# Kernel optimization log

Measured on AMD Instinct MI355X. Metric: run time of the kernel, lower is better.

Reference implementation:

```python
import jax, jax.numpy as jnp
import numpy as np

N = 100000   # nodes
E = 1200000  # edges
D = 64       # feat_dim == num_hidden
G = 64       # graphs in batch
EPS = 1e-5   # BatchNorm eps


def setup_inputs() -> dict:
    key = jax.random.key(0)
    ks = jax.random.split(key, 24)
    inp = {}
    inp['x'] = jax.random.normal(ks[0], (N, D), jnp.float32)
    inp['edge_index'] = jax.random.randint(ks[1], (2, E), 0, N, dtype=jnp.int32)
    inp['batch'] = jnp.sort(jax.random.randint(ks[2], (N,), 0, G, dtype=jnp.int32))
    s = 1.0 / np.sqrt(D)
    for i, kw in zip(range(1, 4), ks[3:6]):
        inp[f'W{i}'] = jax.random.normal(kw, (D, D), jnp.float32) * s
    for i, kb in zip(range(1, 4), ks[6:9]):
        inp[f'b{i}'] = jax.random.normal(kb, (D,), jnp.float32) * 0.02
    for i, base in zip(range(1, 3), (9, 13)):
        inp[f'g{i}'] = 1.0 + 0.1 * jax.random.normal(ks[base], (D,), jnp.float32)
        inp[f'be{i}'] = 0.1 * jax.random.normal(ks[base + 1], (D,), jnp.float32)
        inp[f'rm{i}'] = 0.1 * jax.random.normal(ks[base + 2], (D,), jnp.float32)
        inp[f'rv{i}'] = jax.random.uniform(ks[base + 3], (D,), jnp.float32, 0.5, 1.5)
    return inp


def _gcn_conv(x, W, b, src, dst, n):
    # PyG GCNConv: h = X W; symmetric normalization with self-loops; scatter-add; + bias
    h = x @ W
    deg = jax.ops.segment_sum(jnp.ones((src.shape[0],), h.dtype), dst, num_segments=n) + 1.0
    dis = jax.lax.rsqrt(deg)                          # deg >= 1 from self loop
    msg = (dis[src] * dis[dst])[:, None] * h[src]     # [E, D] gather + normalize
    out = jax.ops.segment_sum(msg, dst, num_segments=n)
    out = out + (dis * dis)[:, None] * h              # self-loop contribution
    return out + b


def _bn(x, g, be, rm, rv):
    # BatchNorm1d in eval mode (running stats)
    return (x - rm) * jax.lax.rsqrt(rv + EPS) * g + be


def reference(x, edge_index, batch, W1, b1, W2, b2, W3, b3,
              g1, be1, rm1, rv1, g2, be2, rm2, rv2):
    src, dst = edge_index[0], edge_index[1]
    h = jax.nn.relu(_bn(_gcn_conv(x, W1, b1, src, dst, N), g1, be1, rm1, rv1))
    h = jax.nn.relu(_bn(_gcn_conv(h, W2, b2, src, dst, N), g2, be2, rm2, rv2))
    h = _gcn_conv(h, W3, b3, src, dst, N)
    # global mean pool over graphs
    counts = jax.ops.segment_sum(jnp.ones((N,), h.dtype), batch, num_segments=G)
    sums = jax.ops.segment_sum(h, batch, num_segments=G)
    hg = sums / jnp.maximum(counts, 1.0)[:, None]
    return (h, hg)
```

## Files before the change

### kernel.cpp

```cpp
#include <hip/hip_runtime.h>
#include <hip/hip_fp16.h>

#define D 64
#define EPS 1e-5f

#define BK_SHIFT 9
#define BK_W 512
#define NBMAX 256
#define BK_CAP 8192
#define CHUNK 4096

typedef _Float16 h8v __attribute__((ext_vector_type(8)));
typedef float f4v __attribute__((ext_vector_type(4)));


__global__ __launch_bounds__(256) void bucket_k(const int* __restrict__ src,
                                                const int* __restrict__ dst,
                                                int* __restrict__ bcnt,
                                                int* __restrict__ pairs,
                                                int e, int nbk) {
  __shared__ int hcnt[NBMAX];
  __shared__ int hbase[NBMAX];
  const int t = threadIdx.x;
  const int e0 = blockIdx.x * CHUNK;
  const int e1 = min(e0 + CHUNK, e);
  for (int i = t; i < nbk; i += 256) hcnt[i] = 0;
  __syncthreads();
  for (int i = e0 + t; i < e1; i += 256)
    atomicAdd(&hcnt[dst[i] >> BK_SHIFT], 1);
  __syncthreads();
  for (int i = t; i < nbk; i += 256) {
    int c = hcnt[i];
    hbase[i] = c ? atomicAdd(&bcnt[i], c) : 0;
    hcnt[i] = 0;
  }
  __syncthreads();
  for (int i = e0 + t; i < e1; i += 256) {
    int s = src[i], d = dst[i];
    int b = d >> BK_SHIFT;
    int r = hbase[b] + atomicAdd(&hcnt[b], 1);
    if (r < BK_CAP) pairs[(size_t)b * BK_CAP + r] = (s << BK_SHIFT) | (d & (BK_W - 1));
  }
}


__global__ __launch_bounds__(256) void bucket2csr_k(const int* __restrict__ bcnt,
                                                    const int* __restrict__ pairs,
                                                    int2* __restrict__ rpdeg,
                                                    float* __restrict__ dis,
                                                    int* __restrict__ col, int n) {
  __shared__ int h[BK_W];
  __shared__ int cur[BK_W];
  __shared__ int s1[256], s2[256];
  __shared__ int stage[BK_CAP];
  const int b = blockIdx.x, t = threadIdx.x;
  const int base = b << BK_SHIFT;
  const int slab0 = b * BK_CAP;
  const int m = min(bcnt[b], BK_CAP);

  h[t] = 0; h[t + 256] = 0;
  for (int i = t; i < BK_CAP; i += 256) stage[i] = 0;
  __syncthreads();
  const int* p = pairs + (size_t)b * BK_CAP;
  for (int i = t; i < m; i += 256) atomicAdd(&h[p[i] & (BK_W - 1)], 1);
  __syncthreads();

  const int pc1 = (h[t] + 3) & ~3;
  const int pc2 = (h[t + 256] + 3) & ~3;
  s1[t] = pc1; s2[t] = pc2;
  __syncthreads();
  for (int off = 1; off < 256; off <<= 1) {
    int x1 = (t >= off) ? s1[t - off] : 0;
    int x2 = (t >= off) ? s2[t - off] : 0;
    __syncthreads();
    s1[t] += x1; s2[t] += x2;
    __syncthreads();
  }
  const int tot1 = s1[255];
  const int mpad = tot1 + s2[255];
  cur[t]       = s1[t] - pc1;
  cur[t + 256] = tot1 + s2[t] - pc2;
  {
    int n1 = base + t, n2 = base + t + 256;
    if (n1 < n) { rpdeg[n1] = make_int2(slab0 + cur[t], h[t]);
                  dis[n1] = rsqrtf((float)h[t] + 1.0f); }
    if (n2 < n) { rpdeg[n2] = make_int2(slab0 + cur[t + 256], h[t + 256]);
                  dis[n2] = rsqrtf((float)h[t + 256] + 1.0f); }
  }
  __syncthreads();

  for (int i = t; i < m; i += 256) {
    int pk = p[i];
    int r = atomicAdd(&cur[pk & (BK_W - 1)], 1);
    stage[r] = pk >> BK_SHIFT;
  }
  __syncthreads();
  const int mout = min(mpad + 16, BK_CAP);
  for (int i = t; i < mout; i += 256) col[slab0 + i] = stage[i];
}


__global__ __launch_bounds__(256) void setup_k(const float* __restrict__ W1,
                                               const float* __restrict__ W2,
                                               const float* __restrict__ W3,
                                               const float* __restrict__ b1,
                                               const float* __restrict__ b2,
                                               const float* __restrict__ b3,
                                               const float* __restrict__ g1, const float* __restrict__ be1,
                                               const float* __restrict__ rm1, const float* __restrict__ rv1,
                                               const float* __restrict__ g2, const float* __restrict__ be2,
                                               const float* __restrict__ rm2, const float* __restrict__ rv2,
                                               _Float16* __restrict__ Wt1,
                                               _Float16* __restrict__ Wt2,
                                               _Float16* __restrict__ Wt3,
                                               float* __restrict__ scsh,
                                               int* __restrict__ zbase, int zwords,
                                               unsigned int* __restrict__ hzrowA,
                                               unsigned int* __restrict__ hzrowB) {
  int gid = blockIdx.x * 256 + threadIdx.x;
  if (gid < zwords) { zbase[gid] = 0; return; }
  gid -= zwords;
  if (gid < 64) {
    if (gid < 32) hzrowA[gid] = 0u; else hzrowB[gid - 32] = 0u;
    return;
  }
  gid -= 64;
  if (gid < 192) {
    int j = gid & 63, l = gid >> 6;
    float sc, sh;
    if (l == 0)      { sc = g1[j] * rsqrtf(rv1[j] + EPS); sh = (b1[j] - rm1[j]) * sc + be1[j]; }
    else if (l == 1) { sc = g2[j] * rsqrtf(rv2[j] + EPS); sh = (b2[j] - rm2[j]) * sc + be2[j]; }
    else             { sc = 1.0f;                          sh = b3[j]; }
    scsh[l * 128 + j] = sc;
    scsh[l * 128 + 64 + j] = sh;
    return;
  }
  gid -= 192;
  if (gid < 3 * 4096) {
    const int mat = gid >> 12, e = gid & 4095;
    const float* Wm = (mat == 0) ? W1 : (mat == 1) ? W2 : W3;
    _Float16* Wt    = (mat == 0) ? Wt1 : (mat == 1) ? Wt2 : Wt3;
    const int k = e >> 6, j = e & 63;
    Wt[j * 64 + k] = (_Float16)Wm[e];
  }
}


template <typename InT>
__global__ __launch_bounds__(256) void gemm_k(const InT* __restrict__ in,
                                              const _Float16* __restrict__ Wt,
                                              const float* __restrict__ dis,
                                              __half* __restrict__ out, int nrows) {
  const int lane = threadIdx.x & 63;
  const int w    = threadIdx.x >> 6;
  const int t16  = lane & 15;
  const int q    = lane >> 4;
  const int rb   = blockIdx.x * 64 + w * 16;
  if (rb >= nrows) return;

  h8v bf[4][2];
#pragma unroll
  for (int cg = 0; cg < 4; ++cg) {
    const _Float16* wp = Wt + (cg * 16 + t16) * 64 + q * 8;
    bf[cg][0] = *(const h8v*)(wp);
    bf[cg][1] = *(const h8v*)(wp + 32);
  }

  const int ar = min(rb + t16, nrows - 1);
  h8v a0, a1;
  if constexpr (sizeof(InT) == 2) {
    const _Float16* ap = (const _Float16*)in + (size_t)ar * D + q * 8;
    a0 = *(const h8v*)(ap);
    a1 = *(const h8v*)(ap + 32);
  } else {
    const float* ap = (const float*)in + (size_t)ar * D + q * 8;
    const float4 l0 = *(const float4*)(ap);
    const float4 h0 = *(const float4*)(ap + 4);
    const float4 l1 = *(const float4*)(ap + 32);
    const float4 h1 = *(const float4*)(ap + 36);
    a0[0] = (_Float16)l0.x; a0[1] = (_Float16)l0.y; a0[2] = (_Float16)l0.z; a0[3] = (_Float16)l0.w;
    a0[4] = (_Float16)h0.x; a0[5] = (_Float16)h0.y; a0[6] = (_Float16)h0.z; a0[7] = (_Float16)h0.w;
    a1[0] = (_Float16)l1.x; a1[1] = (_Float16)l1.y; a1[2] = (_Float16)l1.z; a1[3] = (_Float16)l1.w;
    a1[4] = (_Float16)h1.x; a1[5] = (_Float16)h1.y; a1[6] = (_Float16)h1.z; a1[7] = (_Float16)h1.w;
  }

  f4v acc0 = {0.f, 0.f, 0.f, 0.f};
  f4v acc1 = acc0, acc2 = acc0, acc3 = acc0;
  acc0 = __builtin_amdgcn_mfma_f32_16x16x32_f16(a0, bf[0][0], acc0, 0, 0, 0);
  acc1 = __builtin_amdgcn_mfma_f32_16x16x32_f16(a0, bf[1][0], acc1, 0, 0, 0);
  acc2 = __builtin_amdgcn_mfma_f32_16x16x32_f16(a0, bf[2][0], acc2, 0, 0, 0);
  acc3 = __builtin_amdgcn_mfma_f32_16x16x32_f16(a0, bf[3][0], acc3, 0, 0, 0);
  acc0 = __builtin_amdgcn_mfma_f32_16x16x32_f16(a1, bf[0][1], acc0, 0, 0, 0);
  acc1 = __builtin_amdgcn_mfma_f32_16x16x32_f16(a1, bf[1][1], acc1, 0, 0, 0);
  acc2 = __builtin_amdgcn_mfma_f32_16x16x32_f16(a1, bf[2][1], acc2, 0, 0, 0);
  acc3 = __builtin_amdgcn_mfma_f32_16x16x32_f16(a1, bf[3][1], acc3, 0, 0, 0);

  const float4 dv = *(const float4*)&dis[rb + q * 4];
  _Float16* oh = (_Float16*)out;
#pragma unroll
  for (int r = 0; r < 4; ++r) {
    const int row = rb + q * 4 + r;
    if (row < nrows) {
      const float dsc = (&dv.x)[r];
      _Float16* op = oh + (size_t)row * D + t16;
      op[0]  = (_Float16)(dsc * acc0[r]);
      op[16] = (_Float16)(dsc * acc1[r]);
      op[32] = (_Float16)(dsc * acc2[r]);
      op[48] = (_Float16)(dsc * acc3[r]);
    }
  }
}


template <bool RELU, typename OutT>
__global__ __launch_bounds__(256) void agg_k(const __half* __restrict__ h2s,
                                             const int2* __restrict__ rpdeg,
                                             const int* __restrict__ col,
                                             const float* __restrict__ dis,
                                             const float* __restrict__ scsh,
                                             OutT* __restrict__ out, int n) {
  const int lane = threadIdx.x & 63;
  const int wv   = (blockIdx.x * blockDim.x + threadIdx.x) >> 6;
  const int nb   = __builtin_amdgcn_readfirstlane(wv * 4);
  if (nb >= n) return;
  const int g  = lane >> 4;
  const int sl = lane & 15;
  const int jb = 4 * g;
  const uint2* __restrict__ h2v = (const uint2*)h2s;

  int nd[4], p[4], dg[4];
#pragma unroll
  for (int i = 0; i < 4; ++i) nd[i] = min(nb + i, n - 1);
#pragma unroll
  for (int i = 0; i < 4; ++i) { int2 rd = rpdeg[nd[i]]; p[i] = rd.x; dg[i] = rd.y; }

  uint2 self[4];
  int4  cc[4];
#pragma unroll
  for (int i = 0; i < 4; ++i) {
    self[i] = h2v[(size_t)nd[i] * 16 + sl];
    cc[i]   = *(const int4*)&col[p[i] + jb];
  }

  const __half2 zero2 = __floats2half2_rn(0.f, 0.f);
  const uint2 zz = make_uint2(0u, 0u);
  __half2 acc[4][4];
#pragma unroll
  for (int i = 0; i < 4; ++i)
#pragma unroll
    for (int s = 0; s < 4; ++s) acc[i][s] = zero2;

#pragma unroll
  for (int i = 0; i < 4; ++i) {
    uint2 r0 = h2v[(size_t)cc[i].x * 16 + sl];
    uint2 r1 = h2v[(size_t)cc[i].y * 16 + sl];
    uint2 r2 = h2v[(size_t)cc[i].z * 16 + sl];
    uint2 r3 = h2v[(size_t)cc[i].w * 16 + sl];
    r0 = (jb + 0 < dg[i]) ? r0 : zz;  r1 = (jb + 1 < dg[i]) ? r1 : zz;
    r2 = (jb + 2 < dg[i]) ? r2 : zz;  r3 = (jb + 3 < dg[i]) ? r3 : zz;
    acc[i][0] = __hadd2(acc[i][0], *(const __half2*)&r0.x);
    acc[i][1] = __hadd2(acc[i][1], *(const __half2*)&r0.y);
    acc[i][2] = __hadd2(acc[i][2], *(const __half2*)&r1.x);
    acc[i][3] = __hadd2(acc[i][3], *(const __half2*)&r1.y);
    acc[i][0] = __hadd2(acc[i][0], *(const __half2*)&r2.x);
    acc[i][1] = __hadd2(acc[i][1], *(const __half2*)&r2.y);
    acc[i][2] = __hadd2(acc[i][2], *(const __half2*)&r3.x);
    acc[i][3] = __hadd2(acc[i][3], *(const __half2*)&r3.y);
  }

#pragma unroll
  for (int i = 0; i < 4; ++i) {
    for (int e = 16; e < dg[i]; e += 16) {
      const int4 c2 = *(const int4*)&col[p[i] + e + jb];
      uint2 r0 = h2v[(size_t)c2.x * 16 + sl];
      uint2 r1 = h2v[(size_t)c2.y * 16 + sl];
      uint2 r2 = h2v[(size_t)c2.z * 16 + sl];
      uint2 r3 = h2v[(size_t)c2.w * 16 + sl];
      const int j = e + jb;
      r0 = (j + 0 < dg[i]) ? r0 : zz;  r1 = (j + 1 < dg[i]) ? r1 : zz;
      r2 = (j + 2 < dg[i]) ? r2 : zz;  r3 = (j + 3 < dg[i]) ? r3 : zz;
      acc[i][0] = __hadd2(acc[i][0], *(const __half2*)&r0.x);
      acc[i][1] = __hadd2(acc[i][1], *(const __half2*)&r0.y);
      acc[i][2] = __hadd2(acc[i][2], *(const __half2*)&r1.x);
      acc[i][3] = __hadd2(acc[i][3], *(const __half2*)&r1.y);
      acc[i][0] = __hadd2(acc[i][0], *(const __half2*)&r2.x);
      acc[i][1] = __hadd2(acc[i][1], *(const __half2*)&r2.y);
      acc[i][2] = __hadd2(acc[i][2], *(const __half2*)&r3.x);
      acc[i][3] = __hadd2(acc[i][3], *(const __half2*)&r3.y);
    }
  }

  const float4 sc = *(const float4*)&scsh[4 * sl];
  const float4 sh = *(const float4*)&scsh[64 + 4 * sl];

#pragma unroll
  for (int i = 0; i < 4; ++i) {
    const float2 a0 = __half22float2(acc[i][0]);
    const float2 a1 = __half22float2(acc[i][1]);
    const float2 a2 = __half22float2(acc[i][2]);
    const float2 a3 = __half22float2(acc[i][3]);
    const float2 s0f = __half22float2(*(const __half2*)&self[i].x);
    const float2 s1f = __half22float2(*(const __half2*)&self[i].y);
    float r0 = (a0.x + a2.x) + (g == 0 ? s0f.x : 0.f);
    float r1 = (a0.y + a2.y) + (g == 0 ? s0f.y : 0.f);
    float r2 = (a1.x + a3.x) + (g == 0 ? s1f.x : 0.f);
    float r3 = (a1.y + a3.y) + (g == 0 ? s1f.y : 0.f);
    r0 += __shfl_xor(r0, 16, 64); r1 += __shfl_xor(r1, 16, 64);
    r2 += __shfl_xor(r2, 16, 64); r3 += __shfl_xor(r3, 16, 64);
    r0 += __shfl_xor(r0, 32, 64); r1 += __shfl_xor(r1, 32, 64);
    r2 += __shfl_xor(r2, 32, 64); r3 += __shfl_xor(r3, 32, 64);
    const float di = dis[nd[i]];
    float o0 = fmaf(di * r0, sc.x, sh.x);
    float o1 = fmaf(di * r1, sc.y, sh.y);
    float o2 = fmaf(di * r2, sc.z, sh.z);
    float o3 = fmaf(di * r3, sc.w, sh.w);
    if (RELU) {
      o0 = fmaxf(o0, 0.f); o1 = fmaxf(o1, 0.f);
      o2 = fmaxf(o2, 0.f); o3 = fmaxf(o3, 0.f);
    }
    if (g == 0 && nb + i < n) {
      if constexpr (sizeof(OutT) == 2) {
        union { __half2 h[2]; uint2 u; } v;
        v.h[0] = __floats2half2_rn(o0, o1);
        v.h[1] = __floats2half2_rn(o2, o3);
        *(uint2*)&out[(size_t)nd[i] * D + 4 * sl] = v.u;
      } else {
        *(float4*)&out[(size_t)nd[i] * D + 4 * sl] = make_float4(o0, o1, o2, o3);
      }
    }
  }
}


template <bool RELU>
__global__ __launch_bounds__(256) void aggemm_k(const __half* __restrict__ h2s,
                                                const int2* __restrict__ rpdeg,
                                                const int* __restrict__ col,
                                                const float* __restrict__ dis,
                                                const float* __restrict__ scsh,
                                                const _Float16* __restrict__ Wt,
                                                __half* __restrict__ out, int n) {
  __shared__ _Float16 ylds[16][72];
  const int lane = threadIdx.x & 63;
  const int w    = threadIdx.x >> 6;
  const int nb   = __builtin_amdgcn_readfirstlane(blockIdx.x * 16 + w * 4);
  const int g  = lane >> 4;
  const int sl = lane & 15;
  const int jb = 4 * g;
  const uint2* __restrict__ h2v = (const uint2*)h2s;

  int nd[4], p[4], dg[4];
#pragma unroll
  for (int i = 0; i < 4; ++i) nd[i] = min(nb + i, n - 1);
#pragma unroll
  for (int i = 0; i < 4; ++i) { int2 rd = rpdeg[nd[i]]; p[i] = rd.x; dg[i] = rd.y; }

  uint2 self[4];
  int4  cc[4];
#pragma unroll
  for (int i = 0; i < 4; ++i) {
    self[i] = h2v[(size_t)nd[i] * 16 + sl];
    cc[i]   = *(const int4*)&col[p[i] + jb];
  }

  const __half2 zero2 = __floats2half2_rn(0.f, 0.f);
  const uint2 zz = make_uint2(0u, 0u);
  __half2 acc[4][4];
#pragma unroll
  for (int i = 0; i < 4; ++i)
#pragma unroll
    for (int s = 0; s < 4; ++s) acc[i][s] = zero2;

#pragma unroll
  for (int i = 0; i < 4; ++i) {
    uint2 r0 = h2v[(size_t)cc[i].x * 16 + sl];
    uint2 r1 = h2v[(size_t)cc[i].y * 16 + sl];
    uint2 r2 = h2v[(size_t)cc[i].z * 16 + sl];
    uint2 r3 = h2v[(size_t)cc[i].w * 16 + sl];
    r0 = (jb + 0 < dg[i]) ? r0 : zz;  r1 = (jb + 1 < dg[i]) ? r1 : zz;
    r2 = (jb + 2 < dg[i]) ? r2 : zz;  r3 = (jb + 3 < dg[i]) ? r3 : zz;
    acc[i][0] = __hadd2(acc[i][0], *(const __half2*)&r0.x);
    acc[i][1] = __hadd2(acc[i][1], *(const __half2*)&r0.y);
    acc[i][2] = __hadd2(acc[i][2], *(const __half2*)&r1.x);
    acc[i][3] = __hadd2(acc[i][3], *(const __half2*)&r1.y);
    acc[i][0] = __hadd2(acc[i][0], *(const __half2*)&r2.x);
    acc[i][1] = __hadd2(acc[i][1], *(const __half2*)&r2.y);
    acc[i][2] = __hadd2(acc[i][2], *(const __half2*)&r3.x);
    acc[i][3] = __hadd2(acc[i][3], *(const __half2*)&r3.y);
  }

#pragma unroll
  for (int i = 0; i < 4; ++i) {
    for (int e = 16; e < dg[i]; e += 16) {
      const int4 c2 = *(const int4*)&col[p[i] + e + jb];
      uint2 r0 = h2v[(size_t)c2.x * 16 + sl];
      uint2 r1 = h2v[(size_t)c2.y * 16 + sl];
      uint2 r2 = h2v[(size_t)c2.z * 16 + sl];
      uint2 r3 = h2v[(size_t)c2.w * 16 + sl];
      const int j = e + jb;
      r0 = (j + 0 < dg[i]) ? r0 : zz;  r1 = (j + 1 < dg[i]) ? r1 : zz;
      r2 = (j + 2 < dg[i]) ? r2 : zz;  r3 = (j + 3 < dg[i]) ? r3 : zz;
      acc[i][0] = __hadd2(acc[i][0], *(const __half2*)&r0.x);
      acc[i][1] = __hadd2(acc[i][1], *(const __half2*)&r0.y);
      acc[i][2] = __hadd2(acc[i][2], *(const __half2*)&r1.x);
      acc[i][3] = __hadd2(acc[i][3], *(const __half2*)&r1.y);
      acc[i][0] = __hadd2(acc[i][0], *(const __half2*)&r2.x);
      acc[i][1] = __hadd2(acc[i][1], *(const __half2*)&r2.y);
      acc[i][2] = __hadd2(acc[i][2], *(const __half2*)&r3.x);
      acc[i][3] = __hadd2(acc[i][3], *(const __half2*)&r3.y);
    }
  }

  const float4 sc = *(const float4*)&scsh[4 * sl];
  const float4 sh = *(const float4*)&scsh[64 + 4 * sl];

#pragma unroll
  for (int i = 0; i < 4; ++i) {
    const float2 a0 = __half22float2(acc[i][0]);
    const float2 a1 = __half22float2(acc[i][1]);
    const float2 a2 = __half22float2(acc[i][2]);
    const float2 a3 = __half22float2(acc[i][3]);
    const float2 s0f = __half22float2(*(const __half2*)&self[i].x);
    const float2 s1f = __half22float2(*(const __half2*)&self[i].y);
    float r0 = (a0.x + a2.x) + (g == 0 ? s0f.x : 0.f);
    float r1 = (a0.y + a2.y) + (g == 0 ? s0f.y : 0.f);
    float r2 = (a1.x + a3.x) + (g == 0 ? s1f.x : 0.f);
    float r3 = (a1.y + a3.y) + (g == 0 ? s1f.y : 0.f);
    r0 += __shfl_xor(r0, 16, 64); r1 += __shfl_xor(r1, 16, 64);
    r2 += __shfl_xor(r2, 16, 64); r3 += __shfl_xor(r3, 16, 64);
    r0 += __shfl_xor(r0, 32, 64); r1 += __shfl_xor(r1, 32, 64);
    r2 += __shfl_xor(r2, 32, 64); r3 += __shfl_xor(r3, 32, 64);
    const float di = dis[nd[i]];
    float o0 = fmaf(di * r0, sc.x, sh.x);
    float o1 = fmaf(di * r1, sc.y, sh.y);
    float o2 = fmaf(di * r2, sc.z, sh.z);
    float o3 = fmaf(di * r3, sc.w, sh.w);
    if (RELU) {
      o0 = fmaxf(o0, 0.f); o1 = fmaxf(o1, 0.f);
      o2 = fmaxf(o2, 0.f); o3 = fmaxf(o3, 0.f);
    }
    if (g == 0) {
      union { __half2 h[2]; uint2 u; } v;
      v.h[0] = __floats2half2_rn(o0, o1);
      v.h[1] = __floats2half2_rn(o2, o3);
      *(uint2*)&ylds[w * 4 + i][4 * sl] = v.u;
    }
  }

  __syncthreads();

  {
    const h8v a0 = *(const h8v*)&ylds[sl][g * 8];
    const h8v a1 = *(const h8v*)&ylds[sl][g * 8 + 32];
    const _Float16* wp = Wt + (w * 16 + sl) * 64 + g * 8;
    const h8v b0 = *(const h8v*)(wp);
    const h8v b1 = *(const h8v*)(wp + 32);
    f4v ga = {0.f, 0.f, 0.f, 0.f};
    ga = __builtin_amdgcn_mfma_f32_16x16x32_f16(a0, b0, ga, 0, 0, 0);
    ga = __builtin_amdgcn_mfma_f32_16x16x32_f16(a1, b1, ga, 0, 0, 0);

    const int rb = blockIdx.x * 16;
    const float4 dv = *(const float4*)&dis[rb + g * 4];
    _Float16* oh = (_Float16*)out;
#pragma unroll
    for (int r = 0; r < 4; ++r) {
      const int row = rb + g * 4 + r;
      if (row < n) {
        const float dsc = (&dv.x)[r];
        oh[(size_t)row * D + w * 16 + sl] = (_Float16)(dsc * ga[r]);
      }
    }
  }
}


__global__ __launch_bounds__(256) void pool_k(const float* __restrict__ h,
                                              const int* __restrict__ batch,
                                              float* __restrict__ psum,
                                              float* __restrict__ pcnt, int n) {
  int lane  = threadIdx.x & 63;
  int wid   = __builtin_amdgcn_readfirstlane((blockIdx.x * blockDim.x + threadIdx.x) >> 6);
  int start = wid * 64;
  if (start >= n) return;
  int end = min(start + 64, n);
  int cur = batch[start];
  float sum = 0.f;
  int run = 0;
  for (int i = start; i < end; ++i) {
    int g = batch[i];
    if (g != cur) {
      atomicAdd(&psum[cur * D + lane], sum);
      if (lane == 0) atomicAdd(&pcnt[cur], (float)run);
      sum = 0.f; run = 0; cur = g;
    }
    sum += h[(size_t)i * D + lane];
    run += 1;
  }
  atomicAdd(&psum[cur * D + lane], sum);
  if (lane == 0) atomicAdd(&pcnt[cur], (float)run);
}

__global__ void pooldiv_k(const float* __restrict__ psum, const float* __restrict__ pcnt,
                          float* __restrict__ hg) {
  int t = blockIdx.x * blockDim.x + threadIdx.x;
  if (t < 64 * D) hg[t] = psum[t] / fmaxf(pcnt[t >> 6], 1.0f);
}


extern "C" void kernel_launch(void* const* d_in, const int* in_sizes, int n_in,
                              void* d_out, int out_size, void* d_ws, size_t ws_size,
                              hipStream_t stream) {
  const float* x   = (const float*)d_in[0];
  const int*   ei  = (const int*)d_in[1];
  const int*   bat = (const int*)d_in[2];
  const float* W1  = (const float*)d_in[3];
  const float* W2  = (const float*)d_in[4];
  const float* W3  = (const float*)d_in[5];
  const float* b1  = (const float*)d_in[6];
  const float* b2  = (const float*)d_in[7];
  const float* b3  = (const float*)d_in[8];
  const float* g1  = (const float*)d_in[9];
  const float* be1 = (const float*)d_in[10];
  const float* rm1 = (const float*)d_in[11];
  const float* rv1 = (const float*)d_in[12];
  const float* g2  = (const float*)d_in[13];
  const float* be2 = (const float*)d_in[14];
  const float* rm2 = (const float*)d_in[15];
  const float* rv2 = (const float*)d_in[16];

  const int n = in_sizes[0] / D;
  const int e = in_sizes[1] / 2;
  const int* src = ei;
  const int* dst = ei + e;
  const int nbk = (n + BK_W - 1) >> BK_SHIFT;

  char* ws = (char*)d_ws;
  size_t off = 0;
  auto alloc = [&](size_t bytes) -> void* {
    void* p = ws + off;
    off = (off + bytes + 255) & ~(size_t)255;
    return p;
  };
  __half*   hbufB = (__half*)alloc((size_t)(n + 1) * D * 2);
  int*      pairs = (int*)alloc((size_t)NBMAX * BK_CAP * 4);
  __half*   hbufA = (__half*)alloc((size_t)(n + 1) * D * 2);
  int2*     rpdeg = (int2*)alloc((size_t)(n + 1) * 8);
  float*    dis   = (float*)alloc((size_t)(n + 16) * 4);
  int*      col   = (int*)alloc((size_t)NBMAX * BK_CAP * 4);
  float*    scsh  = (float*)alloc(6 * 64 * 4);
  _Float16* Wt1   = (_Float16*)alloc(4096 * 2);
  _Float16* Wt2   = (_Float16*)alloc(4096 * 2);
  _Float16* Wt3   = (_Float16*)alloc(4096 * 2);
  int*      bcnt  = (int*)alloc(NBMAX * 4);
  float*    psum  = (float*)alloc(64 * D * 4);
  float*    pcnt  = (float*)alloc(64 * 4);
  const int zwords = (int)((((char*)pcnt + 64 * 4) - (char*)bcnt) / 4);

  float* hout = (float*)d_out;
  float* hg   = (float*)d_out + (size_t)n * D;

  const int setup_items = zwords + 64 + 192 + 3 * 4096;
  setup_k<<<(setup_items + 255) / 256, 256, 0, stream>>>(
      W1, W2, W3, b1, b2, b3, g1, be1, rm1, rv1, g2, be2, rm2, rv2,
      Wt1, Wt2, Wt3, scsh, bcnt, zwords,
      (unsigned int*)(hbufA + (size_t)n * D),
      (unsigned int*)(hbufB + (size_t)n * D));

  bucket_k<<<(e + CHUNK - 1) / CHUNK, 256, 0, stream>>>(src, dst, bcnt, pairs, e, nbk);
  bucket2csr_k<<<nbk, 256, 0, stream>>>(bcnt, pairs, rpdeg, dis, col, n);

  const int gemm_blocks = (n + 63) / 64;
  const int fuse_blocks = (n + 15) / 16;
  const int agg_waves   = (n + 3) / 4;
  const int agg_blocks  = (agg_waves * 64 + 255) / 256;

  gemm_k<float><<<gemm_blocks, 256, 0, stream>>>(x, Wt1, dis, hbufA, n);
  aggemm_k<true><<<fuse_blocks, 256, 0, stream>>>(hbufA, rpdeg, col, dis, scsh + 0 * 128, Wt2, hbufB, n);
  aggemm_k<true><<<fuse_blocks, 256, 0, stream>>>(hbufB, rpdeg, col, dis, scsh + 1 * 128, Wt3, hbufA, n);
  agg_k<false, float><<<agg_blocks, 256, 0, stream>>>(hbufA, rpdeg, col, dis, scsh + 2 * 128, hout, n);

  const int pool_waves = (n + 63) / 64;
  pool_k<<<(pool_waves * 64 + 255) / 256, 256, 0, stream>>>(hout, bat, psum, pcnt, n);
  pooldiv_k<<<(64 * D + 255) / 256, 256, 0, stream>>>(psum, pcnt, hg);
}
```

Measured before the change: 278.7 us.

## Fuse mean-pool into final aggregation and prefetch two neighbor chunks up front

The separate pool kernel is removed. The final aggregation kernel now accumulates per-graph partial sums from its outputs in registers and flushes them with atomics, so the float output no longer has to be re-read. Both aggregation kernels now issue the first 32 neighbor gathers before any accumulation, redirecting padded slots to a zero row at index n instead of masking loaded values. This raises memory-level parallelism but also register pressure, and it makes more atomic calls per wave, since each wave covers 4 nodes instead of 64.

```diff
diff --git a/kernel.cpp b/kernel.cpp
--- a/kernel.cpp
+++ b/kernel.cpp
@@ -212,17 +212,19 @@
 }
 
 
-template <bool RELU, typename OutT>
-__global__ __launch_bounds__(256) void agg_k(const __half* __restrict__ h2s,
-                                             const int2* __restrict__ rpdeg,
-                                             const int* __restrict__ col,
-                                             const float* __restrict__ dis,
-                                             const float* __restrict__ scsh,
-                                             OutT* __restrict__ out, int n) {
+
+template <bool RELU>
+__global__ __launch_bounds__(256) void aggemm_k(const __half* __restrict__ h2s,
+                                                const int2* __restrict__ rpdeg,
+                                                const int* __restrict__ col,
+                                                const float* __restrict__ dis,
+                                                const float* __restrict__ scsh,
+                                                const _Float16* __restrict__ Wt,
+                                                __half* __restrict__ out, int n) {
+  __shared__ _Float16 ylds[16][72];
   const int lane = threadIdx.x & 63;
-  const int wv   = (blockIdx.x * blockDim.x + threadIdx.x) >> 6;
-  const int nb   = __builtin_amdgcn_readfirstlane(wv * 4);
-  if (nb >= n) return;
+  const int w    = threadIdx.x >> 6;
+  const int nb   = __builtin_amdgcn_readfirstlane(blockIdx.x * 16 + w * 4);
   const int g  = lane >> 4;
   const int sl = lane & 15;
   const int jb = 4 * g;
@@ -234,59 +236,92 @@
 #pragma unroll
   for (int i = 0; i < 4; ++i) { int2 rd = rpdeg[nd[i]]; p[i] = rd.x; dg[i] = rd.y; }
 
+  int4 c1[4], c2[4];
+#pragma unroll
+  for (int i = 0; i < 4; ++i) c1[i] = *(const int4*)&col[p[i] + jb];
+#pragma unroll
+  for (int i = 0; i < 4; ++i) c2[i] = *(const int4*)&col[p[i] + 16 + jb];
+#pragma unroll
+  for (int i = 0; i < 4; ++i) {
+    c1[i].x = (jb + 0  < dg[i]) ? c1[i].x : n;
+    c1[i].y = (jb + 1  < dg[i]) ? c1[i].y : n;
+    c1[i].z = (jb + 2  < dg[i]) ? c1[i].z : n;
+    c1[i].w = (jb + 3  < dg[i]) ? c1[i].w : n;
+    c2[i].x = (jb + 16 < dg[i]) ? c2[i].x : n;
+    c2[i].y = (jb + 17 < dg[i]) ? c2[i].y : n;
+    c2[i].z = (jb + 18 < dg[i]) ? c2[i].z : n;
+    c2[i].w = (jb + 19 < dg[i]) ? c2[i].w : n;
+  }
+
+  uint2 r[4][4], s[4][4];
+#pragma unroll
+  for (int i = 0; i < 4; ++i) {
+    r[i][0] = h2v[(size_t)c1[i].x * 16 + sl];
+    r[i][1] = h2v[(size_t)c1[i].y * 16 + sl];
+    r[i][2] = h2v[(size_t)c1[i].z * 16 + sl];
+    r[i][3] = h2v[(size_t)c1[i].w * 16 + sl];
+  }
+#pragma unroll
+  for (int i = 0; i < 4; ++i) {
+    s[i][0] = h2v[(size_t)c2[i].x * 16 + sl];
+    s[i][1] = h2v[(size_t)c2[i].y * 16 + sl];
+    s[i][2] = h2v[(size_t)c2[i].z * 16 + sl];
+    s[i][3] = h2v[(size_t)c2[i].w * 16 + sl];
+  }
   uint2 self[4];
-  int4  cc[4];
-#pragma unroll
-  for (int i = 0; i < 4; ++i) {
-    self[i] = h2v[(size_t)nd[i] * 16 + sl];
-    cc[i]   = *(const int4*)&col[p[i] + jb];
-  }
-
-  const __half2 zero2 = __floats2half2_rn(0.f, 0.f);
-  const uint2 zz = make_uint2(0u, 0u);
+#pragma unroll
+  for (int i = 0; i < 4; ++i) self[i] = h2v[(size_t)nd[i] * 16 + sl];
+
   __half2 acc[4][4];
 #pragma unroll
   for (int i = 0; i < 4; ++i)
 #pragma unroll
-    for (int s = 0; s < 4; ++s) acc[i][s] = zero2;
-
-#pragma unroll
-  for (int i = 0; i < 4; ++i) {
-    uint2 r0 = h2v[(size_t)cc[i].x * 16 + sl];
-    uint2 r1 = h2v[(size_t)cc[i].y * 16 + sl];
-    uint2 r2 = h2v[(size_t)cc[i].z * 16 + sl];
-    uint2 r3 = h2v[(size_t)cc[i].w * 16 + sl];
-    r0 = (jb + 0 < dg[i]) ? r0 : zz;  r1 = (jb + 1 < dg[i]) ? r1 : zz;
-    r2 = (jb + 2 < dg[i]) ? r2 : zz;  r3 = (jb + 3 < dg[i]) ? r3 : zz;
-    acc[i][0] = __hadd2(acc[i][0], *(const __half2*)&r0.x);
-    acc[i][1] = __hadd2(acc[i][1], *(const __half2*)&r0.y);
-    acc[i][2] = __hadd2(acc[i][2], *(const __half2*)&r1.x);
-    acc[i][3] = __hadd2(acc[i][3], *(const __half2*)&r1.y);
-    acc[i][0] = __hadd2(acc[i][0], *(const __half2*)&r2.x);
-    acc[i][1] = __hadd2(acc[i][1], *(const __half2*)&r2.y);
-    acc[i][2] = __hadd2(acc[i][2], *(const __half2*)&r3.x);
-    acc[i][3] = __hadd2(acc[i][3], *(const __half2*)&r3.y);
-  }
-
-#pragma unroll
-  for (int i = 0; i < 4; ++i) {
-    for (int e = 16; e < dg[i]; e += 16) {
-      const int4 c2 = *(const int4*)&col[p[i] + e + jb];
-      uint2 r0 = h2v[(size_t)c2.x * 16 + sl];
-      uint2 r1 = h2v[(size_t)c2.y * 16 + sl];
-      uint2 r2 = h2v[(size_t)c2.z * 16 + sl];
-      uint2 r3 = h2v[(size_t)c2.w * 16 + sl];
+    for (int q2 = 0; q2 < 4; ++q2) acc[i][q2] = __floats2half2_rn(0.f, 0.f);
+
+#pragma unroll
+  for (int i = 0; i < 4; ++i) {
+    acc[i][0] = __hadd2(acc[i][0], *(const __half2*)&r[i][0].x);
+    acc[i][1] = __hadd2(acc[i][1], *(const __half2*)&r[i][0].y);
+    acc[i][2] = __hadd2(acc[i][2], *(const __half2*)&r[i][1].x);
+    acc[i][3] = __hadd2(acc[i][3], *(const __half2*)&r[i][1].y);
+    acc[i][0] = __hadd2(acc[i][0], *(const __half2*)&r[i][2].x);
+    acc[i][1] = __hadd2(acc[i][1], *(const __half2*)&r[i][2].y);
+    acc[i][2] = __hadd2(acc[i][2], *(const __half2*)&r[i][3].x);
+    acc[i][3] = __hadd2(acc[i][3], *(const __half2*)&r[i][3].y);
+  }
+#pragma unroll
+  for (int i = 0; i < 4; ++i) {
+    acc[i][0] = __hadd2(acc[i][0], *(const __half2*)&s[i][0].x);
+    acc[i][1] = __hadd2(acc[i][1], *(const __half2*)&s[i][0].y);
+    acc[i][2] = __hadd2(acc[i][2], *(const __half2*)&s[i][1].x);
+    acc[i][3] = __hadd2(acc[i][3], *(const __half2*)&s[i][1].y);
+    acc[i][0] = __hadd2(acc[i][0], *(const __half2*)&s[i][2].x);
+    acc[i][1] = __hadd2(acc[i][1], *(const __half2*)&s[i][2].y);
+    acc[i][2] = __hadd2(acc[i][2], *(const __half2*)&s[i][3].x);
+    acc[i][3] = __hadd2(acc[i][3], *(const __half2*)&s[i][3].y);
+  }
+
+#pragma unroll
+  for (int i = 0; i < 4; ++i) {
+    for (int e = 32; e < dg[i]; e += 16) {
+      int4 c = *(const int4*)&col[p[i] + e + jb];
       const int j = e + jb;
-      r0 = (j + 0 < dg[i]) ? r0 : zz;  r1 = (j + 1 < dg[i]) ? r1 : zz;
-      r2 = (j + 2 < dg[i]) ? r2 : zz;  r3 = (j + 3 < dg[i]) ? r3 : zz;
-      acc[i][0] = __hadd2(acc[i][0], *(const __half2*)&r0.x);
-      acc[i][1] = __hadd2(acc[i][1], *(const __half2*)&r0.y);
-      acc[i][2] = __hadd2(acc[i][2], *(const __half2*)&r1.x);
-      acc[i][3] = __hadd2(acc[i][3], *(const __half2*)&r1.y);
-      acc[i][0] = __hadd2(acc[i][0], *(const __half2*)&r2.x);
-      acc[i][1] = __hadd2(acc[i][1], *(const __half2*)&r2.y);
-      acc[i][2] = __hadd2(acc[i][2], *(const __half2*)&r3.x);
-      acc[i][3] = __hadd2(acc[i][3], *(const __half2*)&r3.y);
+      c.x = (j + 0 < dg[i]) ? c.x : n;
+      c.y = (j + 1 < dg[i]) ? c.y : n;
+      c.z = (j + 2 < dg[i]) ? c.z : n;
+      c.w = (j + 3 < dg[i]) ? c.w : n;
+      uint2 t0 = h2v[(size_t)c.x * 16 + sl];
+      uint2 t1 = h2v[(size_t)c.y * 16 + sl];
+      uint2 t2 = h2v[(size_t)c.z * 16 + sl];
+      uint2 t3 = h2v[(size_t)c.w * 16 + sl];
+      acc[i][0] = __hadd2(acc[i][0], *(const __half2*)&t0.x);
+      acc[i][1] = __hadd2(acc[i][1], *(const __half2*)&t0.y);
+      acc[i][2] = __hadd2(acc[i][2], *(const __half2*)&t1.x);
+      acc[i][3] = __hadd2(acc[i][3], *(const __half2*)&t1.y);
+      acc[i][0] = __hadd2(acc[i][0], *(const __half2*)&t2.x);
+      acc[i][1] = __hadd2(acc[i][1], *(const __half2*)&t2.y);
+      acc[i][2] = __hadd2(acc[i][2], *(const __half2*)&t3.x);
+      acc[i][3] = __hadd2(acc[i][3], *(const __half2*)&t3.y);
     }
   }
 
@@ -318,32 +353,54 @@
       o0 = fmaxf(o0, 0.f); o1 = fmaxf(o1, 0.f);
       o2 = fmaxf(o2, 0.f); o3 = fmaxf(o3, 0.f);
     }
-    if (g == 0 && nb + i < n) {
-      if constexpr (sizeof(OutT) == 2) {
-        union { __half2 h[2]; uint2 u; } v;
-        v.h[0] = __floats2half2_rn(o0, o1);
-        v.h[1] = __floats2half2_rn(o2, o3);
-        *(uint2*)&out[(size_t)nd[i] * D + 4 * sl] = v.u;
-      } else {
-        *(float4*)&out[(size_t)nd[i] * D + 4 * sl] = make_float4(o0, o1, o2, o3);
+    if (g == 0) {
+      union { __half2 h[2]; uint2 u; } v;
+      v.h[0] = __floats2half2_rn(o0, o1);
+      v.h[1] = __floats2half2_rn(o2, o3);
+      *(uint2*)&ylds[w * 4 + i][4 * sl] = v.u;
+    }
+  }
+
+  __syncthreads();
+
+  {
+    const h8v a0 = *(const h8v*)&ylds[sl][g * 8];
+    const h8v a1 = *(const h8v*)&ylds[sl][g * 8 + 32];
+    const _Float16* wp = Wt + (w * 16 + sl) * 64 + g * 8;
+    const h8v b0 = *(const h8v*)(wp);
+    const h8v b1 = *(const h8v*)(wp + 32);
+    f4v ga = {0.f, 0.f, 0.f, 0.f};
+    ga = __builtin_amdgcn_mfma_f32_16x16x32_f16(a0, b0, ga, 0, 0, 0);
+    ga = __builtin_amdgcn_mfma_f32_16x16x32_f16(a1, b1, ga, 0, 0, 0);
+
+    const int rb = blockIdx.x * 16;
+    const float4 dv = *(const float4*)&dis[rb + g * 4];
+    _Float16* oh = (_Float16*)out;
+#pragma unroll
+    for (int r2_ = 0; r2_ < 4; ++r2_) {
+      const int row = rb + g * 4 + r2_;
+      if (row < n) {
+        const float dsc = (&dv.x)[r2_];
+        oh[(size_t)row * D + w * 16 + sl] = (_Float16)(dsc * ga[r2_]);
       }
     }
   }
 }
 
 
-template <bool RELU>
-__global__ __launch_bounds__(256) void aggemm_k(const __half* __restrict__ h2s,
-                                                const int2* __restrict__ rpdeg,
-                                                const int* __restrict__ col,
-                                                const float* __restrict__ dis,
-                                                const float* __restrict__ scsh,
-                                                const _Float16* __restrict__ Wt,
-                                                __half* __restrict__ out, int n) {
-  __shared__ _Float16 ylds[16][72];
+__global__ __launch_bounds__(256) void aggpool_k(const __half* __restrict__ h2s,
+                                                 const int2* __restrict__ rpdeg,
+                                                 const int* __restrict__ col,
+                                                 const float* __restrict__ dis,
+                                                 const float* __restrict__ scsh,
+                                                 const int* __restrict__ batch,
+                                                 float* __restrict__ out,
+                                                 float* __restrict__ psum,
+                                                 float* __restrict__ pcnt, int n) {
   const int lane = threadIdx.x & 63;
-  const int w    = threadIdx.x >> 6;
-  const int nb   = __builtin_amdgcn_readfirstlane(blockIdx.x * 16 + w * 4);
+  const int wv   = (blockIdx.x * blockDim.x + threadIdx.x) >> 6;
+  const int nb   = __builtin_amdgcn_readfirstlane(wv * 4);
+  if (nb >= n) return;
   const int g  = lane >> 4;
   const int sl = lane & 15;
   const int jb = 4 * g;
@@ -355,64 +412,104 @@
 #pragma unroll
   for (int i = 0; i < 4; ++i) { int2 rd = rpdeg[nd[i]]; p[i] = rd.x; dg[i] = rd.y; }
 
+  int4 c1[4], c2[4];
+#pragma unroll
+  for (int i = 0; i < 4; ++i) c1[i] = *(const int4*)&col[p[i] + jb];
+#pragma unroll
+  for (int i = 0; i < 4; ++i) c2[i] = *(const int4*)&col[p[i] + 16 + jb];
+#pragma unroll
+  for (int i = 0; i < 4; ++i) {
+    c1[i].x = (jb + 0  < dg[i]) ? c1[i].x : n;
+    c1[i].y = (jb + 1  < dg[i]) ? c1[i].y : n;
+    c1[i].z = (jb + 2  < dg[i]) ? c1[i].z : n;
+    c1[i].w = (jb + 3  < dg[i]) ? c1[i].w : n;
+    c2[i].x = (jb + 16 < dg[i]) ? c2[i].x : n;
+    c2[i].y = (jb + 17 < dg[i]) ? c2[i].y : n;
+    c2[i].z = (jb + 18 < dg[i]) ? c2[i].z : n;
+    c2[i].w = (jb + 19 < dg[i]) ? c2[i].w : n;
+  }
+
+  uint2 r[4][4], s[4][4];
+#pragma unroll
+  for (int i = 0; i < 4; ++i) {
+    r[i][0] = h2v[(size_t)c1[i].x * 16 + sl];
+    r[i][1] = h2v[(size_t)c1[i].y * 16 + sl];
+    r[i][2] = h2v[(size_t)c1[i].z * 16 + sl];
+    r[i][3] = h2v[(size_t)c1[i].w * 16 + sl];
+  }
+#pragma unroll
+  for (int i = 0; i < 4; ++i) {
+    s[i][0] = h2v[(size_t)c2[i].x * 16 + sl];
+    s[i][1] = h2v[(size_t)c2[i].y * 16 + sl];
+    s[i][2] = h2v[(size_t)c2[i].z * 16 + sl];
+    s[i][3] = h2v[(size_t)c2[i].w * 16 + sl];
+  }
   uint2 self[4];
-  int4  cc[4];
-#pragma unroll
-  for (int i = 0; i < 4; ++i) {
-    self[i] = h2v[(size_t)nd[i] * 16 + sl];
-    cc[i]   = *(const int4*)&col[p[i] + jb];
-  }
-
-  const __half2 zero2 = __floats2half2_rn(0.f, 0.f);
-  const uint2 zz = make_uint2(0u, 0u);
+#pragma unroll
+  for (int i = 0; i < 4; ++i) self[i] = h2v[(size_t)nd[i] * 16 + sl];
+
   __half2 acc[4][4];
 #pragma unroll
   for (int i = 0; i < 4; ++i)
 #pragma unroll
-    for (int s = 0; s < 4; ++s) acc[i][s] = zero2;
-
-#pragma unroll
-  for (int i = 0; i < 4; ++i) {
-    uint2 r0 = h2v[(size_t)cc[i].x * 16 + sl];
-    uint2 r1 = h2v[(size_t)cc[i].y * 16 + sl];
-    uint2 r2 = h2v[(size_t)cc[i].z * 16 + sl];
-    uint2 r3 = h2v[(size_t)cc[i].w * 16 + sl];
-    r0 = (jb + 0 < dg[i]) ? r0 : zz;  r1 = (jb + 1 < dg[i]) ? r1 : zz;
-    r2 = (jb + 2 < dg[i]) ? r2 : zz;  r3 = (jb + 3 < dg[i]) ? r3 : zz;
-    acc[i][0] = __hadd2(acc[i][0], *(const __half2*)&r0.x);
-    acc[i][1] = __hadd2(acc[i][1], *(const __half2*)&r0.y);
-    acc[i][2] = __hadd2(acc[i][2], *(const __half2*)&r1.x);
-    acc[i][3] = __hadd2(acc[i][3], *(const __half2*)&r1.y);
-    acc[i][0] = __hadd2(acc[i][0], *(const __half2*)&r2.x);
-    acc[i][1] = __hadd2(acc[i][1], *(const __half2*)&r2.y);
-    acc[i][2] = __hadd2(acc[i][2], *(const __half2*)&r3.x);
-    acc[i][3] = __hadd2(acc[i][3], *(const __half2*)&r3.y);
-  }
-
-#pragma unroll
-  for (int i = 0; i < 4; ++i) {
-    for (int e = 16; e < dg[i]; e += 16) {
-      const int4 c2 = *(const int4*)&col[p[i] + e + jb];
-      uint2 r0 = h2v[(size_t)c2.x * 16 + sl];
-      uint2 r1 = h2v[(size_t)c2.y * 16 + sl];
-      uint2 r2 = h2v[(size_t)c2.z * 16 + sl];
-      uint2 r3 = h2v[(size_t)c2.w * 16 + sl];
+    for (int q2 = 0; q2 < 4; ++q2) acc[i][q2] = __floats2half2_rn(0.f, 0.f);
+
+#pragma unroll
+  for (int i = 0; i < 4; ++i) {
+    acc[i][0] = __hadd2(acc[i][0], *(const __half2*)&r[i][0].x);
+    acc[i][1] = __hadd2(acc[i][1], *(const __half2*)&r[i][0].y);
+    acc[i][2] = __hadd2(acc[i][2], *(const __half2*)&r[i][1].x);
+    acc[i][3] = __hadd2(acc[i][3], *(const __half2*)&r[i][1].y);
+    acc[i][0] = __hadd2(acc[i][0], *(const __half2*)&r[i][2].x);
+    acc[i][1] = __hadd2(acc[i][1], *(const __half2*)&r[i][2].y);
+    acc[i][2] = __hadd2(acc[i][2], *(const __half2*)&r[i][3].x);
+    acc[i][3] = __hadd2(acc[i][3], *(const __half2*)&r[i][3].y);
+  }
+#pragma unroll
+  for (int i = 0; i < 4; ++i) {
+    acc[i][0] = __hadd2(acc[i][0], *(const __half2*)&s[i][0].x);
+    acc[i][1] = __hadd2(acc[i][1], *(const __half2*)&s[i][0].y);
+    acc[i][2] = __hadd2(acc[i][2], *(const __half2*)&s[i][1].x);
+    acc[i][3] = __hadd2(acc[i][3], *(const __half2*)&s[i][1].y);
+    acc[i][0] = __hadd2(acc[i][0], *(const __half2*)&s[i][2].x);
+    acc[i][1] = __hadd2(acc[i][1], *(const __half2*)&s[i][2].y);
+    acc[i][2] = __hadd2(acc[i][2], *(const __half2*)&s[i][3].x);
+    acc[i][3] = __hadd2(acc[i][3], *(const __half2*)&s[i][3].y);
+  }
+
+#pragma unroll
+  for (int i = 0; i < 4; ++i) {
+    for (int e = 32; e < dg[i]; e += 16) {
+      int4 c = *(const int4*)&col[p[i] + e + jb];
       const int j = e + jb;
-      r0 = (j + 0 < dg[i]) ? r0 : zz;  r1 = (j + 1 < dg[i]) ? r1 : zz;
-      r2 = (j + 2 < dg[i]) ? r2 : zz;  r3 = (j + 3 < dg[i]) ? r3 : zz;
-      acc[i][0] = __hadd2(acc[i][0], *(const __half2*)&r0.x);
-      acc[i][1] = __hadd2(acc[i][1], *(const __half2*)&r0.y);
-      acc[i][2] = __hadd2(acc[i][2], *(const __half2*)&r1.x);
-      acc[i][3] = __hadd2(acc[i][3], *(const __half2*)&r1.y);
-      acc[i][0] = __hadd2(acc[i][0], *(const __half2*)&r2.x);
-      acc[i][1] = __hadd2(acc[i][1], *(const __half2*)&r2.y);
-      acc[i][2] = __hadd2(acc[i][2], *(const __half2*)&r3.x);
-      acc[i][3] = __hadd2(acc[i][3], *(const __half2*)&r3.y);
-    }
-  }
+      c.x = (j + 0 < dg[i]) ? c.x : n;
+      c.y = (j + 1 < dg[i]) ? c.y : n;
+      c.z = (j + 2 < dg[i]) ? c.z : n;
+      c.w = (j + 3 < dg[i]) ? c.w : n;
+      uint2 t0 = h2v[(size_t)c.x * 16 + sl];
+      uint2 t1 = h2v[(size_t)c.y * 16 + sl];
+      uint2 t2 = h2v[(size_t)c.z * 16 + sl];
+      uint2 t3 = h2v[(size_t)c.w * 16 + sl];
+      acc[i][0] = __hadd2(acc[i][0], *(const __half2*)&t0.x);
+      acc[i][1] = __hadd2(acc[i][1], *(const __half2*)&t0.y);
+      acc[i][2] = __hadd2(acc[i][2], *(const __half2*)&t1.x);
+      acc[i][3] = __hadd2(acc[i][3], *(const __half2*)&t1.y);
+      acc[i][0] = __hadd2(acc[i][0], *(const __half2*)&t2.x);
+      acc[i][1] = __hadd2(acc[i][1], *(const __half2*)&t2.y);
+      acc[i][2] = __hadd2(acc[i][2], *(const __half2*)&t3.x);
+      acc[i][3] = __hadd2(acc[i][3], *(const __half2*)&t3.y);
+    }
+  }
+
+  int bt[4];
+#pragma unroll
+  for (int i = 0; i < 4; ++i) bt[i] = batch[nd[i]];
 
   const float4 sc = *(const float4*)&scsh[4 * sl];
   const float4 sh = *(const float4*)&scsh[64 + 4 * sl];
+
+  float ps0 = 0.f, ps1 = 0.f, ps2 = 0.f, ps3 = 0.f;
+  int cur = bt[0], run = 0;
 
 #pragma unroll
   for (int i = 0; i < 4; ++i) {
@@ -431,73 +528,33 @@
     r0 += __shfl_xor(r0, 32, 64); r1 += __shfl_xor(r1, 32, 64);
     r2 += __shfl_xor(r2, 32, 64); r3 += __shfl_xor(r3, 32, 64);
     const float di = dis[nd[i]];
-    float o0 = fmaf(di * r0, sc.x, sh.x);
-    float o1 = fmaf(di * r1, sc.y, sh.y);
-    float o2 = fmaf(di * r2, sc.z, sh.z);
-    float o3 = fmaf(di * r3, sc.w, sh.w);
-    if (RELU) {
-      o0 = fmaxf(o0, 0.f); o1 = fmaxf(o1, 0.f);
-      o2 = fmaxf(o2, 0.f); o3 = fmaxf(o3, 0.f);
-    }
-    if (g == 0) {
-      union { __half2 h[2]; uint2 u; } v;
-      v.h[0] = __floats2half2_rn(o0, o1);
-      v.h[1] = __floats2half2_rn(o2, o3);
-      *(uint2*)&ylds[w * 4 + i][4 * sl] = v.u;
-    }
-  }
-
-  __syncthreads();
-
-  {
-    const h8v a0 = *(const h8v*)&ylds[sl][g * 8];
-    const h8v a1 = *(const h8v*)&ylds[sl][g * 8 + 32];
-    const _Float16* wp = Wt + (w * 16 + sl) * 64 + g * 8;
-    const h8v b0 = *(const h8v*)(wp);
-    const h8v b1 = *(const h8v*)(wp + 32);
-    f4v ga = {0.f, 0.f, 0.f, 0.f};
-    ga = __builtin_amdgcn_mfma_f32_16x16x32_f16(a0, b0, ga, 0, 0, 0);
-    ga = __builtin_amdgcn_mfma_f32_16x16x32_f16(a1, b1, ga, 0, 0, 0);
-
-    const int rb = blockIdx.x * 16;
-    const float4 dv = *(const float4*)&dis[rb + g * 4];
-    _Float16* oh = (_Float16*)out;
-#pragma unroll
-    for (int r = 0; r < 4; ++r) {
-      const int row = rb + g * 4 + r;
-      if (row < n) {
-        const float dsc = (&dv.x)[r];
-        oh[(size_t)row * D + w * 16 + sl] = (_Float16)(dsc * ga[r]);
+    const float o0 = fmaf(di * r0, sc.x, sh.x);
+    const float o1 = fmaf(di * r1, sc.y, sh.y);
+    const float o2 = fmaf(di * r2, sc.z, sh.z);
+    const float o3 = fmaf(di * r3, sc.w, sh.w);
+    const bool valid = (nb + i < n);
+    if (g == 0 && valid) {
+      *(float4*)&out[(size_t)nd[i] * D + 4 * sl] = make_float4(o0, o1, o2, o3);
+    }
+    if (bt[i] != cur) {
+      if (g == 0) {
+        atomicAdd(&psum[cur * D + 4 * sl + 0], ps0);
+        atomicAdd(&psum[cur * D + 4 * sl + 1], ps1);
+        atomicAdd(&psum[cur * D + 4 * sl + 2], ps2);
+        atomicAdd(&psum[cur * D + 4 * sl + 3], ps3);
+        if (lane == 0) atomicAdd(&pcnt[cur], (float)run);
       }
-    }
-  }
-}
-
-
-__global__ __launch_bounds__(256) void pool_k(const float* __restrict__ h,
-                                              const int* __restrict__ batch,
-                                              float* __restrict__ psum,
-                                              float* __restrict__ pcnt, int n) {
-  int lane  = threadIdx.x & 63;
-  int wid   = __builtin_amdgcn_readfirstlane((blockIdx.x * blockDim.x + threadIdx.x) >> 6);
-  int start = wid * 64;
-  if (start >= n) return;
-  int end = min(start + 64, n);
-  int cur = batch[start];
-  float sum = 0.f;
-  int run = 0;
-  for (int i = start; i < end; ++i) {
-    int g = batch[i];
-    if (g != cur) {
-      atomicAdd(&psum[cur * D + lane], sum);
-      if (lane == 0) atomicAdd(&pcnt[cur], (float)run);
-      sum = 0.f; run = 0; cur = g;
-    }
-    sum += h[(size_t)i * D + lane];
-    run += 1;
-  }
-  atomicAdd(&psum[cur * D + lane], sum);
-  if (lane == 0) atomicAdd(&pcnt[cur], (float)run);
+      ps0 = ps1 = ps2 = ps3 = 0.f; run = 0; cur = bt[i];
+    }
+    if (valid) { ps0 += o0; ps1 += o1; ps2 += o2; ps3 += o3; run += 1; }
+  }
+  if (g == 0 && run > 0) {
+    atomicAdd(&psum[cur * D + 4 * sl + 0], ps0);
+    atomicAdd(&psum[cur * D + 4 * sl + 1], ps1);
+    atomicAdd(&psum[cur * D + 4 * sl + 2], ps2);
+    atomicAdd(&psum[cur * D + 4 * sl + 3], ps3);
+    if (lane == 0) atomicAdd(&pcnt[cur], (float)run);
+  }
 }
 
 __global__ void pooldiv_k(const float* __restrict__ psum, const float* __restrict__ pcnt,
@@ -545,7 +602,7 @@
   int*      pairs = (int*)alloc((size_t)NBMAX * BK_CAP * 4);
   __half*   hbufA = (__half*)alloc((size_t)(n + 1) * D * 2);
   int2*     rpdeg = (int2*)alloc((size_t)(n + 1) * 8);
-  float*    dis   = (float*)alloc((size_t)(n + 16) * 4);
+  float*    dis   = (float*)alloc((size_t)(n + 32) * 4);
   int*      col   = (int*)alloc((size_t)NBMAX * BK_CAP * 4);
   float*    scsh  = (float*)alloc(6 * 64 * 4);
   _Float16* Wt1   = (_Float16*)alloc(4096 * 2);
@@ -577,9 +634,7 @@
   gemm_k<float><<<gemm_blocks, 256, 0, stream>>>(x, Wt1, dis, hbufA, n);
   aggemm_k<true><<<fuse_blocks, 256, 0, stream>>>(hbufA, rpdeg, col, dis, scsh + 0 * 128, Wt2, hbufB, n);
   aggemm_k<true><<<fuse_blocks, 256, 0, stream>>>(hbufB, rpdeg, col, dis, scsh + 1 * 128, Wt3, hbufA, n);
-  agg_k<false, float><<<agg_blocks, 256, 0, stream>>>(hbufA, rpdeg, col, dis, scsh + 2 * 128, hout, n);
-
-  const int pool_waves = (n + 63) / 64;
-  pool_k<<<(pool_waves * 64 + 255) / 256, 256, 0, stream>>>(hout, bat, psum, pcnt, n);
+  aggpool_k<<<agg_blocks, 256, 0, stream>>>(hbufA, rpdeg, col, dis, scsh + 2 * 128, bat,
+                                            hout, psum, pcnt, n);
   pooldiv_k<<<(64 * D + 255) / 256, 256, 0, stream>>>(psum, pcnt, hg);
 }
```

New measurement: 484.6 us. +73.9%, slower.
